# Optimization experiments

Measured on AMD Instinct MI355X. Metric: run time of the kernel, lower is better.

Reference implementation:

```python
import jax, jax.numpy as jnp
import numpy as np

B, L, D = 8, 2048, 1024
LN_EPS = 1e-5
WKV_EPS = 1e-8


def _ln(x, g, b):
    m = x.mean(-1, keepdims=True)
    v = x.var(-1, keepdims=True)  # biased var, matches torch LayerNorm
    return (x - m) * jax.lax.rsqrt(v + LN_EPS) * g + b


def _shift(x):
    # ZeroPad2d((0,0,1,-1)): x_prev[:, t] = x[:, t-1], x_prev[:, 0] = 0
    return jnp.pad(x, ((0, 0), (1, 0), (0, 0)))[:, :-1]


def _wkv(k, v, time_decay, time_first):
    # Faithful to the torch loop: t=0 uses exp(u + k0); t>0 decays prior state
    # (including the u-boosted first term) by exp(-exp(time_decay)).
    ew = jnp.exp(-jnp.exp(time_decay))  # [D]
    e0 = jnp.exp(time_first + k[:, 0])  # [B, D]
    a0 = e0 * v[:, 0]
    b0 = e0

    def step(carry, kv):
        a, b = carry
        kt, vt = kv
        ek = jnp.exp(kt)
        a = ew * a + ek * vt
        b = ew * b + ek
        return (a, b), a / (b + WKV_EPS)

    xs = (jnp.swapaxes(k[:, 1:], 0, 1), jnp.swapaxes(v[:, 1:], 0, 1))  # [L-1, B, D]
    _, outs = jax.lax.scan(step, (a0, b0), xs)
    out0 = (a0 / (b0 + WKV_EPS))[:, None]  # [B, 1, D]
    return jnp.concatenate([out0, jnp.swapaxes(outs, 0, 1)], axis=1)  # [B, L, D]


def setup_inputs() -> dict:
    key = jax.random.key(0)
    ks = jax.random.split(key, 10)
    s = 1.0 / np.sqrt(D)

    def w(k, shape, scale):
        return jax.random.normal(k, shape, jnp.float32) * scale

    return {
        "x": jax.random.normal(ks[0], (B, L, D), jnp.float32),
        "ln1_g": jnp.ones((D,), jnp.float32),
        "ln1_b": jnp.zeros((D,), jnp.float32),
        "Wk": w(ks[1], (D, D), s),
        "Wv": w(ks[2], (D, D), s),
        "Wr": w(ks[3], (D, D), s),
        "Wo": w(ks[4], (D, D), s),
        "time_decay": w(ks[5], (D,), 0.1),
        "time_first": w(ks[6], (D,), 0.1),
        "mix_k": jnp.full((D,), 0.5, jnp.float32),
        "mix_v": jnp.full((D,), 0.5, jnp.float32),
        "mix_r": jnp.full((D,), 0.5, jnp.float32),
        "ln2_g": jnp.ones((D,), jnp.float32),
        "ln2_b": jnp.zeros((D,), jnp.float32),
        "Wfk": w(ks[7], (D, 4 * D), s),
        "Wfv": w(ks[8], (4 * D, D), 1.0 / np.sqrt(4 * D)),
        "Wfr": w(ks[9], (D, D), s),
    }


def reference(x, ln1_g, ln1_b, Wk, Wv, Wr, Wo, time_decay, time_first,
              mix_k, mix_v, mix_r, ln2_g, ln2_b, Wfk, Wfv, Wfr):
    # --- time mixing ---
    xn = _ln(x, ln1_g, ln1_b)
    xp = _shift(xn)
    k = (xn * mix_k + xp * (1.0 - mix_k)) @ Wk
    v = (xn * mix_v + xp * (1.0 - mix_v)) @ Wv
    r = jax.nn.sigmoid((xn * mix_r + xp * (1.0 - mix_r)) @ Wr)
    wkv = _wkv(k, v, time_decay, time_first)
    x = x + (r * wkv) @ Wo
    # --- channel mixing ---
    yn = _ln(x, ln2_g, ln2_b)
    yp = _shift(yn)
    kk = jnp.square(jax.nn.relu((0.5 * yn + 0.5 * yp) @ Wfk))
    rr = jax.nn.sigmoid(yn @ Wfr)
    return x + rr * (kk @ Wfv)
```

## Files before the change

### kernel.cpp

```cpp
#include <hip/hip_runtime.h>
#include <hip/hip_bf16.h>
#include <stdint.h>

typedef __hip_bfloat16 bf16_t;
typedef __attribute__((ext_vector_type(8))) short bf16x8;
typedef __attribute__((ext_vector_type(4))) float f32x4;

#define DEV static __device__ __forceinline__

constexpr int kBB = 8, kL = 2048, kD = 1024;
constexpr int kM = kBB * kL;
constexpr int kSeg = 32, kP = 64;

DEV float bf2f(unsigned short u) { return __uint_as_float((unsigned)u << 16); }
DEV unsigned short f2bf(float f) {
  unsigned u = __float_as_uint(f);
  return (unsigned short)((u + 0x7fffu + ((u >> 16) & 1u)) >> 16);
}

DEV void gld16(const void* g, void* l) {
  const __attribute__((address_space(1))) unsigned* gp =
      (const __attribute__((address_space(1))) unsigned*)(uintptr_t)g;
  __attribute__((address_space(3))) unsigned* lp =
      (__attribute__((address_space(3))) unsigned*)(unsigned)(uintptr_t)l;
  __builtin_amdgcn_global_load_lds(gp, lp, 16, 0, 0);
}

__global__ __launch_bounds__(256) void k_transpose_cast(
    const float* __restrict__ W, bf16_t* __restrict__ Wt, int R, int C) {
  __shared__ float tile[32][33];
  const int bx = blockIdx.x * 32;
  const int by = blockIdx.y * 32;
  const int tx = threadIdx.x & 31, ty = threadIdx.x >> 5;
#pragma unroll
  for (int i = 0; i < 32; i += 8)
    tile[ty + i][tx] = W[(size_t)(by + ty + i) * C + (bx + tx)];
  __syncthreads();
#pragma unroll
  for (int i = 0; i < 32; i += 8)
    Wt[(size_t)(bx + ty + i) * R + (by + tx)] = __float2bfloat16(tile[tx][ty + i]);
}

__global__ __launch_bounds__(256) void k_ln_stats(
    const float* __restrict__ X, float* __restrict__ mean, float* __restrict__ rstd) {
  const int row = blockIdx.x * 4 + (threadIdx.x >> 6);
  const int lane = threadIdx.x & 63;
  const float4* xr = (const float4*)(X + (size_t)row * kD);
  float s = 0.f, s2 = 0.f;
#pragma unroll
  for (int i = 0; i < 4; ++i) {
    float4 v = xr[lane + 64 * i];
    s += v.x + v.y + v.z + v.w;
    s2 += v.x * v.x + v.y * v.y + v.z * v.z + v.w * v.w;
  }
#pragma unroll
  for (int off = 32; off > 0; off >>= 1) {
    s += __shfl_xor(s, off);
    s2 += __shfl_xor(s2, off);
  }
  if (lane == 0) {
    float m = s * (1.f / kD);
    float var = fmaxf(s2 * (1.f / kD) - m * m, 0.f);
    mean[row] = m;
    rstd[row] = rsqrtf(var + 1e-5f);
  }
}

__global__ __launch_bounds__(256) void k_ln_mix1(
    const float* __restrict__ X, const float* __restrict__ mean, const float* __restrict__ rstd,
    const float* __restrict__ g, const float* __restrict__ be,
    const float* __restrict__ mk, const float* __restrict__ mv, const float* __restrict__ mr,
    bf16_t* __restrict__ ok, bf16_t* __restrict__ ov, bf16_t* __restrict__ orr) {
  const int row = blockIdx.x;
  const int l = row & (kL - 1);
  const int i = threadIdx.x;
  const bool hp = (l != 0);
  const float m0 = mean[row], s0 = rstd[row];
  const float m1 = hp ? mean[row - 1] : 0.f;
  const float s1 = hp ? rstd[row - 1] : 0.f;
  float xa[4], pa[4] = {0.f, 0.f, 0.f, 0.f}, ga[4], ba[4], ka[4], va[4], ra[4];
  *(float4*)xa = ((const float4*)(X + (size_t)row * kD))[i];
  if (hp) *(float4*)pa = ((const float4*)(X + (size_t)(row - 1) * kD))[i];
  *(float4*)ga = ((const float4*)g)[i];
  *(float4*)ba = ((const float4*)be)[i];
  *(float4*)ka = ((const float4*)mk)[i];
  *(float4*)va = ((const float4*)mv)[i];
  *(float4*)ra = ((const float4*)mr)[i];
  ushort4 uk, uv, ur;
  unsigned short* pk = (unsigned short*)&uk;
  unsigned short* pv = (unsigned short*)&uv;
  unsigned short* pr = (unsigned short*)&ur;
#pragma unroll
  for (int c = 0; c < 4; ++c) {
    float xn = (xa[c] - m0) * s0 * ga[c] + ba[c];
    float xp = hp ? (pa[c] - m1) * s1 * ga[c] + ba[c] : 0.f;
    pk[c] = f2bf(xn * ka[c] + xp * (1.f - ka[c]));
    pv[c] = f2bf(xn * va[c] + xp * (1.f - va[c]));
    pr[c] = f2bf(xn * ra[c] + xp * (1.f - ra[c]));
  }
  ((ushort4*)(ok + (size_t)row * kD))[i] = uk;
  ((ushort4*)(ov + (size_t)row * kD))[i] = uv;
  ((ushort4*)(orr + (size_t)row * kD))[i] = ur;
}

__global__ __launch_bounds__(256) void k_ln_mix2(
    const float* __restrict__ X, const float* __restrict__ mean, const float* __restrict__ rstd,
    const float* __restrict__ g, const float* __restrict__ be,
    bf16_t* __restrict__ om, bf16_t* __restrict__ on) {
  const int row = blockIdx.x;
  const int l = row & (kL - 1);
  const int i = threadIdx.x;
  const bool hp = (l != 0);
  const float m0 = mean[row], s0 = rstd[row];
  const float m1 = hp ? mean[row - 1] : 0.f;
  const float s1 = hp ? rstd[row - 1] : 0.f;
  float xa[4], pa[4] = {0.f, 0.f, 0.f, 0.f}, ga[4], ba[4];
  *(float4*)xa = ((const float4*)(X + (size_t)row * kD))[i];
  if (hp) *(float4*)pa = ((const float4*)(X + (size_t)(row - 1) * kD))[i];
  *(float4*)ga = ((const float4*)g)[i];
  *(float4*)ba = ((const float4*)be)[i];
  ushort4 um, un;
  unsigned short* qm = (unsigned short*)&um;
  unsigned short* qn = (unsigned short*)&un;
#pragma unroll
  for (int c = 0; c < 4; ++c) {
    float yn = (xa[c] - m0) * s0 * ga[c] + ba[c];
    float yp = hp ? (pa[c] - m1) * s1 * ga[c] + ba[c] : 0.f;
    qm[c] = f2bf(0.5f * (yn + yp));
    qn[c] = f2bf(yn);
  }
  ((ushort4*)(om + (size_t)row * kD))[i] = um;
  ((ushort4*)(on + (size_t)row * kD))[i] = un;
}

__global__ __launch_bounds__(256) void k_wkv_seg(
    const unsigned short* __restrict__ kq, const unsigned short* __restrict__ vq,
    const float* __restrict__ td, const float* __restrict__ tf,
    float* __restrict__ segA, float* __restrict__ segB) {
  const int d = blockIdx.x * 256 + threadIdx.x;
  const int b = blockIdx.y;
  const int s = blockIdx.z;
  const float ew = __expf(-__expf(td[d]));
  const float uu = (s == 0) ? tf[d] : 0.f;
  const size_t base = ((size_t)b * kL + (size_t)s * kP) * kD + d;
  float a = 0.f, bb = 0.f;
  unsigned short kA[16], vA[16], kB[16], vB[16];
  auto pref = [&](unsigned short* ka, unsigned short* va, int c) {
    const size_t o0 = base + (size_t)c * 16 * kD;
#pragma unroll
    for (int j = 0; j < 16; ++j) {
      ka[j] = kq[o0 + (size_t)j * kD];
      va[j] = vq[o0 + (size_t)j * kD];
    }
  };
  auto comp = [&](const unsigned short* ka, const unsigned short* va, int c) {
#pragma unroll
    for (int j = 0; j < 16; ++j) {
      float kf = bf2f(ka[j]);
      if (s == 0 && c == 0 && j == 0) kf += uu;
      float ek = __expf(kf);
      a = ew * a + ek * bf2f(va[j]);
      bb = ew * bb + ek;
    }
  };
  pref(kA, vA, 0);
  pref(kB, vB, 1); comp(kA, vA, 0);
  pref(kA, vA, 2); comp(kB, vB, 1);
  pref(kB, vB, 3); comp(kA, vA, 2);
  comp(kB, vB, 3);
  const size_t sidx = ((size_t)b * kSeg + s) * kD + d;
  segA[sidx] = a;
  segB[sidx] = bb;
}

__global__ __launch_bounds__(256) void k_wkv_carry(
    const float* __restrict__ td,
    const float* __restrict__ segA, const float* __restrict__ segB,
    float* __restrict__ carA, float* __restrict__ carB) {
  const int d = blockIdx.x * 256 + threadIdx.x;
  const int b = blockIdx.y;
  const float ew = __expf(-__expf(td[d]));
  float ewP = ew;
#pragma unroll
  for (int i = 0; i < 6; ++i) ewP *= ewP;
  float ca = 0.f, cb = 0.f;
#pragma unroll 4
  for (int s = 0; s < kSeg; ++s) {
    const size_t idx = ((size_t)b * kSeg + s) * kD + d;
    carA[idx] = ca;
    carB[idx] = cb;
    ca = ewP * ca + segA[idx];
    cb = ewP * cb + segB[idx];
  }
}

__global__ __launch_bounds__(256) void k_wkv_out(
    const unsigned short* __restrict__ kq, const unsigned short* __restrict__ vq,
    const unsigned short* __restrict__ rq, const float* __restrict__ td,
    const float* __restrict__ tf, const float* __restrict__ carA,
    const float* __restrict__ carB, unsigned short* __restrict__ out) {
  const int d = blockIdx.x * 256 + threadIdx.x;
  const int b = blockIdx.y;
  const int s = blockIdx.z;
  const float ew = __expf(-__expf(td[d]));
  const float uu = (s == 0) ? tf[d] : 0.f;
  const size_t base = ((size_t)b * kL + (size_t)s * kP) * kD + d;
  const size_t sidx = ((size_t)b * kSeg + s) * kD + d;
  float a = carA[sidx], bb = carB[sidx];
  unsigned short kA[16], vA[16], rA[16], kB[16], vB[16], rB[16];
  auto pref = [&](unsigned short* ka, unsigned short* va, unsigned short* ra, int c) {
    const size_t o0 = base + (size_t)c * 16 * kD;
#pragma unroll
    for (int j = 0; j < 16; ++j) {
      ka[j] = kq[o0 + (size_t)j * kD];
      va[j] = vq[o0 + (size_t)j * kD];
      ra[j] = rq[o0 + (size_t)j * kD];
    }
  };
  auto comp = [&](const unsigned short* ka, const unsigned short* va,
                  const unsigned short* ra, int c) {
    const size_t o0 = base + (size_t)c * 16 * kD;
#pragma unroll
    for (int j = 0; j < 16; ++j) {
      float kf = bf2f(ka[j]);
      if (s == 0 && c == 0 && j == 0) kf += uu;
      float ek = __expf(kf);
      a = ew * a + ek * bf2f(va[j]);
      bb = ew * bb + ek;
      float y = a / (bb + 1e-8f);
      float sr = 1.f / (1.f + __expf(-bf2f(ra[j])));
      out[o0 + (size_t)j * kD] = f2bf(sr * y);
    }
  };
  pref(kA, vA, rA, 0);
  pref(kB, vB, rB, 1); comp(kA, vA, rA, 0);
  pref(kA, vA, rA, 2); comp(kB, vB, rB, 1);
  pref(kB, vB, rB, 3); comp(kA, vA, rA, 2);
  comp(kB, vB, rB, 3);
}

template <int EPI>
__global__ __launch_bounds__(512, 2) void gemm256(
    const bf16_t* __restrict__ A0, long strA, int lda,
    const bf16_t* __restrict__ B0, long strB, int ldb,
    bf16_t* __restrict__ Cb0, float* __restrict__ Cf, long strC,
    int N, int K, int nbx,
    const float* __restrict__ addf, const bf16_t* __restrict__ mulb) {
  __shared__ __align__(16) char lds[147456];
  const int z = blockIdx.z;
  const bf16_t* A = A0 + (size_t)z * strA;
  const bf16_t* Bt = B0 + (size_t)z * strB;
  const int nwg = gridDim.x;
  const int wg = (blockIdx.x & 7) * (nwg >> 3) + (blockIdx.x >> 3);
  const int by = wg / nbx, bx = wg - by * nbx;
  const long brow = (long)by * 128;
  const long bcol = (long)bx * 256;
  const int tid = threadIdx.x;
  const int lane = tid & 63;
  const int wr = (tid >> 6) >> 2, wc = (tid >> 6) & 3;

  f32x4 acc[4][4] = {};

  const int trow = tid >> 3;
  const int scol = ((tid & 7) * 16) ^ ((trow & 7) << 4);
  const char* As0 = (const char*)(A + (brow + trow) * (size_t)lda) + scol;
  const char* As1 = As0 + 64L * lda * 2;
  const char* Bs0 = (const char*)(Bt + (bcol + trow) * (size_t)ldb) + scol;
  const char* Bs1 = Bs0 + 64L * ldb * 2;
  const char* Bs2 = Bs0 + 128L * ldb * 2;
  const char* Bs3 = Bs0 + 192L * ldb * 2;

#define STAGE(kt, p)                                   \
  {                                                    \
    const long kb = (long)(kt) * 128;                  \
    char* Ad = lds + (p) * 49152 + tid * 16;           \
    char* Bd = Ad + 16384;                             \
    gld16(As0 + kb, Ad);                               \
    gld16(As1 + kb, Ad + 8192);                        \
    gld16(Bs0 + kb, Bd);                               \
    gld16(Bs1 + kb, Bd + 8192);                        \
    gld16(Bs2 + kb, Bd + 16384);                       \
    gld16(Bs3 + kb, Bd + 24576);                       \
  }

  const int l16 = lane & 15, kq = lane >> 4;
  const int swz = (l16 & 7) << 4;
  const int oS0 = (kq * 16) ^ swz;
  const int oS1 = (64 + kq * 16) ^ swz;
  const int arow = (wr * 64 + l16) * 128;
  const int brl = 16384 + (wc * 64 + l16) * 128;

  bf16x8 aE[4], bE[4], aO[4], bO[4];
  const int NT = K >> 6;

  STAGE(0, 0) STAGE(1, 1) STAGE(2, 2)
  asm volatile("s_waitcnt vmcnt(12)" ::: "memory");
  __builtin_amdgcn_s_barrier();
  {
    const char* Ar = lds + arow;
    const char* Br = lds + brl;
#pragma unroll
    for (int m = 0; m < 4; ++m) aE[m] = *(const bf16x8*)(Ar + m * 2048 + oS0);
#pragma unroll
    for (int n = 0; n < 4; ++n) bE[n] = *(const bf16x8*)(Br + n * 2048 + oS0);
  }

  int cur = 0;
  for (int t = 0; t < NT; ++t) {
    const int nxt = (cur < 2) ? cur + 1 : 0;
    const char* Ac = lds + cur * 49152 + arow;
    const char* Bc = lds + cur * 49152 + brl - 16384 + 16384;
#pragma unroll
    for (int m = 0; m < 4; ++m) aO[m] = *(const bf16x8*)(Ac + m * 2048 + oS1);
#pragma unroll
    for (int n = 0; n < 4; ++n) bO[n] = *(const bf16x8*)(Bc + n * 2048 + oS1);
    __builtin_amdgcn_s_setprio(1);
#pragma unroll
    for (int m = 0; m < 4; ++m)
#pragma unroll
      for (int n = 0; n < 4; ++n)
        acc[m][n] = __builtin_amdgcn_mfma_f32_16x16x32_bf16(aE[m], bE[n], acc[m][n], 0, 0, 0);
    __builtin_amdgcn_s_setprio(0);
    asm volatile("s_waitcnt lgkmcnt(0)" ::: "memory");
    if (t + 2 < NT) {
      asm volatile("s_waitcnt vmcnt(6)" ::: "memory");
    } else {
      asm volatile("s_waitcnt vmcnt(0)" ::: "memory");
    }
    __builtin_amdgcn_s_barrier();
    if (t + 3 < NT) STAGE(t + 3, cur)
    if (t + 1 < NT) {
      const char* An = lds + nxt * 49152 + arow;
      const char* Bn = lds + nxt * 49152 + brl;
#pragma unroll
      for (int m = 0; m < 4; ++m) aE[m] = *(const bf16x8*)(An + m * 2048 + oS0);
#pragma unroll
      for (int n = 0; n < 4; ++n) bE[n] = *(const bf16x8*)(Bn + n * 2048 + oS0);
    }
    __builtin_amdgcn_s_setprio(1);
#pragma unroll
    for (int m = 0; m < 4; ++m)
#pragma unroll
      for (int n = 0; n < 4; ++n)
        acc[m][n] = __builtin_amdgcn_mfma_f32_16x16x32_bf16(aO[m], bO[n], acc[m][n], 0, 0, 0);
    __builtin_amdgcn_s_setprio(0);
    cur = nxt;
  }
#undef STAGE

  bf16_t* Cb = Cb0 + (size_t)z * strC;
  const long orow = brow + wr * 64 + (lane >> 4) * 4;
  const long ocol = bcol + wc * 64 + l16;
#pragma unroll
  for (int m = 0; m < 4; ++m) {
#pragma unroll
    for (int reg = 0; reg < 4; ++reg) {
      const long r = orow + m * 16 + reg;
#pragma unroll
      for (int n = 0; n < 4; ++n) {
        const size_t idx = (size_t)r * N + ocol + n * 16;
        const float v = acc[m][n][reg];
        if constexpr (EPI == 0) {
          Cb[idx] = __float2bfloat16(v);
        } else if constexpr (EPI == 1) {
          Cf[idx] = addf[idx] + v;
        } else if constexpr (EPI == 2) {
          float u = v > 0.f ? v : 0.f;
          Cb[idx] = __float2bfloat16(u * u);
        } else if constexpr (EPI == 3) {
          Cb[idx] = __float2bfloat16(1.f / (1.f + __expf(-v)));
        } else if constexpr (EPI == 4) {
          Cf[idx] = v;
        } else {
          Cf[idx] = addf[idx] + __bfloat162float(mulb[idx]) * (Cf[idx] + v);
        }
      }
    }
  }
}

extern "C" void kernel_launch(void* const* d_in, const int* in_sizes, int n_in,
                              void* d_out, int out_size, void* d_ws, size_t ws_size,
                              hipStream_t stream) {
  const float* x    = (const float*)d_in[0];
  const float* ln1g = (const float*)d_in[1];
  const float* ln1b = (const float*)d_in[2];
  const float* Wk   = (const float*)d_in[3];
  const float* Wv   = (const float*)d_in[4];
  const float* Wr   = (const float*)d_in[5];
  const float* Wo   = (const float*)d_in[6];
  const float* td   = (const float*)d_in[7];
  const float* tf   = (const float*)d_in[8];
  const float* mk   = (const float*)d_in[9];
  const float* mv   = (const float*)d_in[10];
  const float* mr   = (const float*)d_in[11];
  const float* ln2g = (const float*)d_in[12];
  const float* ln2b = (const float*)d_in[13];
  const float* Wfk  = (const float*)d_in[14];
  const float* Wfv  = (const float*)d_in[15];
  const float* Wfr  = (const float*)d_in[16];

  char* ws = (char*)d_ws;
  const size_t MB = 1ull << 20;
  bf16_t* WkT  = (bf16_t*)(ws + 0 * MB);
  bf16_t* WvT  = (bf16_t*)(ws + 2 * MB);
  bf16_t* WrT  = (bf16_t*)(ws + 4 * MB);
  bf16_t* WoT  = (bf16_t*)(ws + 6 * MB);
  bf16_t* WfkT = (bf16_t*)(ws + 8 * MB);
  bf16_t* WfvT = (bf16_t*)(ws + 16 * MB);
  bf16_t* WfrT = (bf16_t*)(ws + 24 * MB);
  float* mean1 = (float*)(ws + 26 * MB);
  float* rstd1 = (float*)(ws + 26 * MB + 65536);
  float* mean2 = (float*)(ws + 26 * MB + 131072);
  float* rstd2 = (float*)(ws + 26 * MB + 196608);
  bf16_t* xk   = (bf16_t*)(ws + 28 * MB);
  bf16_t* xv   = (bf16_t*)(ws + 60 * MB);
  bf16_t* xr   = (bf16_t*)(ws + 92 * MB);
  bf16_t* kbuf = (bf16_t*)(ws + 124 * MB);
  bf16_t* vbuf = (bf16_t*)(ws + 156 * MB);
  bf16_t* rbuf = (bf16_t*)(ws + 188 * MB);
  float*  segA = (float*)(ws + 60 * MB);
  float*  segB = (float*)(ws + 61 * MB);
  float*  carA = (float*)(ws + 62 * MB);
  float*  carB = (float*)(ws + 63 * MB);
  bf16_t* rwkv = (bf16_t*)(ws + 92 * MB);
  float*  x1   = (float*)(ws + 28 * MB);
  bf16_t* rr   = (bf16_t*)(ws + 92 * MB);
  bf16_t* ynb  = (bf16_t*)(ws + 124 * MB);
  bf16_t* kk   = (bf16_t*)(ws + 124 * MB);
  bf16_t* ymix = (bf16_t*)(ws + 188 * MB);
  float*  out  = (float*)d_out;
  const long sX = (long)kM * kD;
  const long sW = (long)kD * kD;

  dim3 blk(256), blkg(512);
  k_transpose_cast<<<dim3(32, 32), blk, 0, stream>>>(Wk, WkT, 1024, 1024);
  k_transpose_cast<<<dim3(32, 32), blk, 0, stream>>>(Wv, WvT, 1024, 1024);
  k_transpose_cast<<<dim3(32, 32), blk, 0, stream>>>(Wr, WrT, 1024, 1024);
  k_transpose_cast<<<dim3(32, 32), blk, 0, stream>>>(Wo, WoT, 1024, 1024);
  k_transpose_cast<<<dim3(128, 32), blk, 0, stream>>>(Wfk, WfkT, 1024, 4096);
  k_transpose_cast<<<dim3(32, 128), blk, 0, stream>>>(Wfv, WfvT, 4096, 1024);
  k_transpose_cast<<<dim3(32, 32), blk, 0, stream>>>(Wfr, WfrT, 1024, 1024);

  k_ln_stats<<<kM / 4, blk, 0, stream>>>(x, mean1, rstd1);
  k_ln_mix1<<<kM, blk, 0, stream>>>(x, mean1, rstd1, ln1g, ln1b, mk, mv, mr, xk, xv, xr);
  gemm256<0><<<dim3(512, 1, 3), blkg, 0, stream>>>(xk, sX, 1024, WkT, sW, 1024,
      kbuf, nullptr, sX, 1024, 1024, 4, nullptr, nullptr);
  k_wkv_seg<<<dim3(4, 8, kSeg), blk, 0, stream>>>((const unsigned short*)kbuf,
      (const unsigned short*)vbuf, td, tf, segA, segB);
  k_wkv_carry<<<dim3(4, 8), blk, 0, stream>>>(td, segA, segB, carA, carB);
  k_wkv_out<<<dim3(4, 8, kSeg), blk, 0, stream>>>((const unsigned short*)kbuf,
      (const unsigned short*)vbuf, (const unsigned short*)rbuf, td, tf, carA, carB,
      (unsigned short*)rwkv);
  gemm256<1><<<512, blkg, 0, stream>>>(rwkv, 0, 1024, WoT, 0, 1024,
      nullptr, x1, 0, 1024, 1024, 4, x, nullptr);

  k_ln_stats<<<kM / 4, blk, 0, stream>>>(x1, mean2, rstd2);
  k_ln_mix2<<<kM, blk, 0, stream>>>(x1, mean2, rstd2, ln2g, ln2b, ymix, ynb);
  gemm256<3><<<512, blkg, 0, stream>>>(ynb, 0, 1024, WfrT, 0, 1024,
      rr, nullptr, 0, 1024, 1024, 4, nullptr, nullptr);
  for (int c = 0; c < 2; ++c) {
    gemm256<2><<<1024, blkg, 0, stream>>>(ymix, 0, 1024, WfkT + (size_t)c * 2048 * 1024, 0, 1024,
        kk, nullptr, 0, 2048, 1024, 8, nullptr, nullptr);
    if (c == 0)
      gemm256<4><<<512, blkg, 0, stream>>>(kk, 0, 2048, WfvT + 0, 0, 4096,
          nullptr, out, 0, 1024, 2048, 4, nullptr, nullptr);
    else
      gemm256<6><<<512, blkg, 0, stream>>>(kk, 0, 2048, WfvT + 2048, 0, 4096,
          nullptr, out, 0, 1024, 2048, 4, x1, rr);
  }
}
```

Before: 728.3 us.

## Enlarge GEMM block tile to 256x256 with double-buffered LDS

Changes the GEMM block tile from 128x256 to 256x256, doubling per-wave accumulators to 8x4 MFMA tiles and halving the launch grids. The LDS pipeline drops from three stages to two, with a full vmcnt(0) wait at each iteration. This aims to raise data reuse per loaded byte and cut global/LDS traffic per FLOP. It risks more register pressure and less latency hiding from the shallower prefetch.

Result: faster. 654.1 us (-10.2%).

```diff
diff --git a/kernel.cpp b/kernel.cpp
--- a/kernel.cpp
+++ b/kernel.cpp
@@ -240,119 +240,109 @@
 }
 
 template <int EPI>
-__global__ __launch_bounds__(512, 2) void gemm256(
+__global__ __launch_bounds__(512, 2) void gemmT(
     const bf16_t* __restrict__ A0, long strA, int lda,
     const bf16_t* __restrict__ B0, long strB, int ldb,
     bf16_t* __restrict__ Cb0, float* __restrict__ Cf, long strC,
     int N, int K, int nbx,
     const float* __restrict__ addf, const bf16_t* __restrict__ mulb) {
-  __shared__ __align__(16) char lds[147456];
+  __shared__ __align__(16) char lds[131072];
   const int z = blockIdx.z;
   const bf16_t* A = A0 + (size_t)z * strA;
   const bf16_t* Bt = B0 + (size_t)z * strB;
   const int nwg = gridDim.x;
   const int wg = (blockIdx.x & 7) * (nwg >> 3) + (blockIdx.x >> 3);
   const int by = wg / nbx, bx = wg - by * nbx;
-  const long brow = (long)by * 128;
+  const long brow = (long)by * 256;
   const long bcol = (long)bx * 256;
   const int tid = threadIdx.x;
   const int lane = tid & 63;
-  const int wr = (tid >> 6) >> 2, wc = (tid >> 6) & 3;
-
-  f32x4 acc[4][4] = {};
+  const int wid = tid >> 6;
+  const int wr = wid >> 2, wc = wid & 3;
+
+  f32x4 acc[8][4] = {};
 
   const int trow = tid >> 3;
   const int scol = ((tid & 7) * 16) ^ ((trow & 7) << 4);
-  const char* As0 = (const char*)(A + (brow + trow) * (size_t)lda) + scol;
-  const char* As1 = As0 + 64L * lda * 2;
-  const char* Bs0 = (const char*)(Bt + (bcol + trow) * (size_t)ldb) + scol;
-  const char* Bs1 = Bs0 + 64L * ldb * 2;
-  const char* Bs2 = Bs0 + 128L * ldb * 2;
-  const char* Bs3 = Bs0 + 192L * ldb * 2;
+  const char* Ag = (const char*)(A + (brow + trow) * (size_t)lda) + scol;
+  const char* Bg = (const char*)(Bt + (bcol + trow) * (size_t)ldb) + scol;
+  const long rsA = 64L * lda * 2;
+  const long rsB = 64L * ldb * 2;
 
 #define STAGE(kt, p)                                   \
   {                                                    \
     const long kb = (long)(kt) * 128;                  \
-    char* Ad = lds + (p) * 49152 + tid * 16;           \
-    char* Bd = Ad + 16384;                             \
-    gld16(As0 + kb, Ad);                               \
-    gld16(As1 + kb, Ad + 8192);                        \
-    gld16(Bs0 + kb, Bd);                               \
-    gld16(Bs1 + kb, Bd + 8192);                        \
-    gld16(Bs2 + kb, Bd + 16384);                       \
-    gld16(Bs3 + kb, Bd + 24576);                       \
+    char* Ld = lds + (p) * 65536 + tid * 16;           \
+    gld16(Ag + kb, Ld);                                \
+    gld16(Ag + kb + rsA, Ld + 8192);                   \
+    gld16(Ag + kb + 2 * rsA, Ld + 16384);              \
+    gld16(Ag + kb + 3 * rsA, Ld + 24576);              \
+    gld16(Bg + kb, Ld + 32768);                        \
+    gld16(Bg + kb + rsB, Ld + 40960);                  \
+    gld16(Bg + kb + 2 * rsB, Ld + 49152);              \
+    gld16(Bg + kb + 3 * rsB, Ld + 57344);              \
   }
 
   const int l16 = lane & 15, kq = lane >> 4;
   const int swz = (l16 & 7) << 4;
   const int oS0 = (kq * 16) ^ swz;
   const int oS1 = (64 + kq * 16) ^ swz;
-  const int arow = (wr * 64 + l16) * 128;
-  const int brl = 16384 + (wc * 64 + l16) * 128;
-
-  bf16x8 aE[4], bE[4], aO[4], bO[4];
+  const char* Arow = lds + (wr * 128 + l16) * 128;
+  const char* Brow = lds + 32768 + (wc * 64 + l16) * 128;
+
+  bf16x8 aE[8], bE[4], aO[8], bO[4];
   const int NT = K >> 6;
 
-  STAGE(0, 0) STAGE(1, 1) STAGE(2, 2)
-  asm volatile("s_waitcnt vmcnt(12)" ::: "memory");
+  STAGE(0, 0) STAGE(1, 1)
+  asm volatile("s_waitcnt vmcnt(8)" ::: "memory");
   __builtin_amdgcn_s_barrier();
-  {
-    const char* Ar = lds + arow;
-    const char* Br = lds + brl;
-#pragma unroll
-    for (int m = 0; m < 4; ++m) aE[m] = *(const bf16x8*)(Ar + m * 2048 + oS0);
-#pragma unroll
-    for (int n = 0; n < 4; ++n) bE[n] = *(const bf16x8*)(Br + n * 2048 + oS0);
-  }
-
-  int cur = 0;
+#pragma unroll
+  for (int m = 0; m < 8; ++m) aE[m] = *(const bf16x8*)(Arow + m * 2048 + oS0);
+#pragma unroll
+  for (int n = 0; n < 4; ++n) bE[n] = *(const bf16x8*)(Brow + n * 2048 + oS0);
+
   for (int t = 0; t < NT; ++t) {
-    const int nxt = (cur < 2) ? cur + 1 : 0;
-    const char* Ac = lds + cur * 49152 + arow;
-    const char* Bc = lds + cur * 49152 + brl - 16384 + 16384;
-#pragma unroll
-    for (int m = 0; m < 4; ++m) aO[m] = *(const bf16x8*)(Ac + m * 2048 + oS1);
-#pragma unroll
-    for (int n = 0; n < 4; ++n) bO[n] = *(const bf16x8*)(Bc + n * 2048 + oS1);
+    const int p = t & 1;
+    const char* Ap = Arow + p * 65536;
+    const char* Bp = Brow + p * 65536;
+#pragma unroll
+    for (int m = 0; m < 8; ++m) aO[m] = *(const bf16x8*)(Ap + m * 2048 + oS1);
+#pragma unroll
+    for (int n = 0; n < 4; ++n) bO[n] = *(const bf16x8*)(Bp + n * 2048 + oS1);
     __builtin_amdgcn_s_setprio(1);
 #pragma unroll
-    for (int m = 0; m < 4; ++m)
+    for (int m = 0; m < 8; ++m)
 #pragma unroll
       for (int n = 0; n < 4; ++n)
         acc[m][n] = __builtin_amdgcn_mfma_f32_16x16x32_bf16(aE[m], bE[n], acc[m][n], 0, 0, 0);
     __builtin_amdgcn_s_setprio(0);
     asm volatile("s_waitcnt lgkmcnt(0)" ::: "memory");
-    if (t + 2 < NT) {
-      asm volatile("s_waitcnt vmcnt(6)" ::: "memory");
-    } else {
-      asm volatile("s_waitcnt vmcnt(0)" ::: "memory");
-    }
+    asm volatile("s_waitcnt vmcnt(0)" ::: "memory");
     __builtin_amdgcn_s_barrier();
-    if (t + 3 < NT) STAGE(t + 3, cur)
+    if (t + 2 < NT) STAGE(t + 2, p)
     if (t + 1 < NT) {
-      const char* An = lds + nxt * 49152 + arow;
-      const char* Bn = lds + nxt * 49152 + brl;
-#pragma unroll
-      for (int m = 0; m < 4; ++m) aE[m] = *(const bf16x8*)(An + m * 2048 + oS0);
+      const char* An = Arow + (1 - p) * 65536;
+      const char* Bn = Brow + (1 - p) * 65536;
+#pragma unroll
+      for (int m = 0; m < 8; ++m) aE[m] = *(const bf16x8*)(An + m * 2048 + oS0);
 #pragma unroll
       for (int n = 0; n < 4; ++n) bE[n] = *(const bf16x8*)(Bn + n * 2048 + oS0);
     }
     __builtin_amdgcn_s_setprio(1);
 #pragma unroll
-    for (int m = 0; m < 4; ++m)
+    for (int m = 0; m < 8; ++m)
 #pragma unroll
       for (int n = 0; n < 4; ++n)
         acc[m][n] = __builtin_amdgcn_mfma_f32_16x16x32_bf16(aO[m], bO[n], acc[m][n], 0, 0, 0);
     __builtin_amdgcn_s_setprio(0);
-    cur = nxt;
   }
 #undef STAGE
 
   bf16_t* Cb = Cb0 + (size_t)z * strC;
-  const long orow = brow + wr * 64 + (lane >> 4) * 4;
+  const long orow = brow + wr * 128 + (lane >> 4) * 4;
   const long ocol = bcol + wc * 64 + l16;
 #pragma unroll
-  for (int m = 0; m < 4; ++m) {
+  for (int m = 0; m < 8; ++m) {
 #pragma unroll
     for (int reg = 0; reg < 4; ++reg) {
       const long r = orow + m * 16 + reg;
@@ -444,7 +434,7 @@
 
   k_ln_stats<<<kM / 4, blk, 0, stream>>>(x, mean1, rstd1);
   k_ln_mix1<<<kM, blk, 0, stream>>>(x, mean1, rstd1, ln1g, ln1b, mk, mv, mr, xk, xv, xr);
-  gemm256<0><<<dim3(512, 1, 3), blkg, 0, stream>>>(xk, sX, 1024, WkT, sW, 1024,
+  gemmT<0><<<dim3(256, 1, 3), blkg, 0, stream>>>(xk, sX, 1024, WkT, sW, 1024,
       kbuf, nullptr, sX, 1024, 1024, 4, nullptr, nullptr);
   k_wkv_seg<<<dim3(4, 8, kSeg), blk, 0, stream>>>((const unsigned short*)kbuf,
       (const unsigned short*)vbuf, td, tf, segA, segB);
@@ -452,21 +442,21 @@
   k_wkv_out<<<dim3(4, 8, kSeg), blk, 0, stream>>>((const unsigned short*)kbuf,
       (const unsigned short*)vbuf, (const unsigned short*)rbuf, td, tf, carA, carB,
       (unsigned short*)rwkv);
-  gemm256<1><<<512, blkg, 0, stream>>>(rwkv, 0, 1024, WoT, 0, 1024,
+  gemmT<1><<<256, blkg, 0, stream>>>(rwkv, 0, 1024, WoT, 0, 1024,
       nullptr, x1, 0, 1024, 1024, 4, x, nullptr);
 
   k_ln_stats<<<kM / 4, blk, 0, stream>>>(x1, mean2, rstd2);
   k_ln_mix2<<<kM, blk, 0, stream>>>(x1, mean2, rstd2, ln2g, ln2b, ymix, ynb);
-  gemm256<3><<<512, blkg, 0, stream>>>(ynb, 0, 1024, WfrT, 0, 1024,
+  gemmT<3><<<256, blkg, 0, stream>>>(ynb, 0, 1024, WfrT, 0, 1024,
       rr, nullptr, 0, 1024, 1024, 4, nullptr, nullptr);
   for (int c = 0; c < 2; ++c) {
-    gemm256<2><<<1024, blkg, 0, stream>>>(ymix, 0, 1024, WfkT + (size_t)c * 2048 * 1024, 0, 1024,
+    gemmT<2><<<512, blkg, 0, stream>>>(ymix, 0, 1024, WfkT + (size_t)c * 2048 * 1024, 0, 1024,
         kk, nullptr, 0, 2048, 1024, 8, nullptr, nullptr);
     if (c == 0)
-      gemm256<4><<<512, blkg, 0, stream>>>(kk, 0, 2048, WfvT + 0, 0, 4096,
+      gemmT<4><<<256, blkg, 0, stream>>>(kk, 0, 2048, WfvT + 0, 0, 4096,
           nullptr, out, 0, 1024, 2048, 4, nullptr, nullptr);
     else
-      gemm256<6><<<512, blkg, 0, stream>>>(kk, 0, 2048, WfvT + 2048, 0, 4096,
+      gemmT<6><<<256, blkg, 0, stream>>>(kk, 0, 2048, WfvT + 2048, 0, 4096,
           nullptr, out, 0, 1024, 2048, 4, x1, rr);
   }
 }
```
